# Kernel optimization log

Measured on AMD Instinct MI355X. Metric: run time of the kernel, lower is better.

The kernel has to match this reference:

```python
import jax, jax.numpy as jnp
import numpy as np

B, S, D = 2, 2048, 2048
NH, NKV = 32, 8
HD = D // NH          # 64
NREP = NH // NKV      # 4


def _rope(x, cos, sin):
    # x: [B, S, H, HD]; cos/sin: [S, HD//2]
    x2 = x.reshape(*x.shape[:-1], HD // 2, 2)
    x0, x1 = x2[..., 0], x2[..., 1]
    c = cos[None, :, None, :]
    s = sin[None, :, None, :]
    r0 = x0 * c - x1 * s
    r1 = x0 * s + x1 * c
    return jnp.stack([r0, r1], axis=-1).reshape(x.shape)


def setup_inputs() -> dict:
    key = jax.random.key(0)
    ks = jax.random.split(key, 5)
    x = jax.random.normal(ks[0], (B, S, D), dtype=jnp.float32)
    wq = jax.random.normal(ks[1], (D, NH * HD), dtype=jnp.float32) * (D ** -0.5)
    wk = jax.random.normal(ks[2], (D, NKV * HD), dtype=jnp.float32) * (D ** -0.5)
    wv = jax.random.normal(ks[3], (D, NKV * HD), dtype=jnp.float32) * (D ** -0.5)
    wo = jax.random.normal(ks[4], (NH * HD, D), dtype=jnp.float32) * (D ** -0.5)
    # standard RoPE frequencies: theta = 10000^(-2i/HD)
    inv_freq = 1.0 / (10000.0 ** (np.arange(0, HD, 2, dtype=np.float32) / HD))
    angles = np.arange(S, dtype=np.float32)[:, None] * inv_freq[None, :]  # [S, HD/2]
    freqs_cos = jnp.asarray(np.cos(angles))
    freqs_sin = jnp.asarray(np.sin(angles))
    return {"x": x, "freqs_cos": freqs_cos, "freqs_sin": freqs_sin,
            "wq": wq, "wk": wk, "wv": wv, "wo": wo}


def reference(x, freqs_cos, freqs_sin, wq, wk, wv, wo):
    b, s, _ = x.shape
    xq = (x @ wq).reshape(b, s, NH, HD)
    xk = (x @ wk).reshape(b, s, NKV, HD)
    xv = (x @ wv).reshape(b, s, NKV, HD)
    xq = _rope(xq, freqs_cos, freqs_sin)
    xk = _rope(xk, freqs_cos, freqs_sin)
    # GQA repeat_kv: expand kv heads to NH
    keys = jnp.repeat(xk, NREP, axis=2)    # [B, S, NH, HD]
    values = jnp.repeat(xv, NREP, axis=2)
    scores = jnp.einsum('bqhd,bkhd->bhqk', xq, keys) / jnp.sqrt(jnp.float32(HD))
    causal = jnp.tril(jnp.ones((s, s), dtype=bool))
    scores = jnp.where(causal[None, None], scores, -jnp.inf)
    attn = jax.nn.softmax(scores.astype(jnp.float32), axis=-1).astype(xq.dtype)
    out = jnp.einsum('bhqk,bkhd->bqhd', attn, values).reshape(b, s, NH * HD)
    return out @ wo
```

## Files before the change

kernel.cpp:

```cpp
#include <hip/hip_runtime.h>
#include <hip/hip_bf16.h>

#define S_LEN 2048
#define DMODEL 2048
#define N_H 32
#define N_KV 8
#define H_D 64
#define ROWS 4096
#define QKV_LD 3072

typedef __bf16 bf16x8 __attribute__((ext_vector_type(8)));
typedef float f32x4 __attribute__((ext_vector_type(4)));

static __device__ __forceinline__ unsigned short f2bf(float f) {
  unsigned int u = __float_as_uint(f);
  u += 0x7FFFu + ((u >> 16) & 1u);
  return (unsigned short)(u >> 16);
}
static __device__ __forceinline__ unsigned short f2bf_tr(float f) {
  return (unsigned short)(__float_as_uint(f) >> 16);
}
static __device__ __forceinline__ float bf2f(unsigned short s) {
  return __uint_as_float((unsigned int)s << 16);
}

static __device__ __forceinline__ void async16(const void* g, void* l) {
  __builtin_amdgcn_global_load_lds(
      (const __attribute__((address_space(1))) unsigned int*)g,
      (__attribute__((address_space(3))) unsigned int*)l, 16, 0, 0);
}

__global__ __launch_bounds__(256) void cvt_bf16_k(
    const float* __restrict__ in, unsigned short* __restrict__ out) {
  const size_t i = ((size_t)blockIdx.x * 256 + threadIdx.x) * 8;
  const float4 a = *(const float4*)&in[i];
  const float4 b = *(const float4*)&in[i + 4];
  union { unsigned short u[8]; uint4 v; } p;
  p.u[0] = f2bf(a.x); p.u[1] = f2bf(a.y); p.u[2] = f2bf(a.z); p.u[3] = f2bf(a.w);
  p.u[4] = f2bf(b.x); p.u[5] = f2bf(b.y); p.u[6] = f2bf(b.z); p.u[7] = f2bf(b.w);
  *(uint4*)&out[i] = p.v;
}

__global__ __launch_bounds__(256) void prep_all_k(
    const float* __restrict__ x, const float* __restrict__ wq,
    const float* __restrict__ wk, const float* __restrict__ wv,
    const float* __restrict__ wo, unsigned short* __restrict__ xb,
    unsigned short* __restrict__ wqkvT, unsigned short* __restrict__ woT) {
  const int z = blockIdx.z;
  if (z == 4) {
    const size_t i =
        (((size_t)blockIdx.y * 64 + blockIdx.x) * 256 + threadIdx.x) * 8;
    const float4 a = *(const float4*)&x[i];
    const float4 b = *(const float4*)&x[i + 4];
    union { unsigned short u[8]; uint4 v; } p;
    p.u[0] = f2bf(a.x); p.u[1] = f2bf(a.y); p.u[2] = f2bf(a.z); p.u[3] = f2bf(a.w);
    p.u[4] = f2bf(b.x); p.u[5] = f2bf(b.y); p.u[6] = f2bf(b.z); p.u[7] = f2bf(b.w);
    *(uint4*)&xb[i] = p.v;
    return;
  }
  const float* in;
  unsigned short* out;
  int C;
  if (z == 0)      { in = wq; out = wqkvT;                  C = 2048; }
  else if (z == 1) { in = wk; out = wqkvT + 2048ull * 2048; C = 512;  }
  else if (z == 2) { in = wv; out = wqkvT + 2560ull * 2048; C = 512;  }
  else             { in = wo; out = woT;                    C = 2048; }
  if (blockIdx.x * 32 >= C) return;

  __shared__ unsigned short tile[32][33];
  const int tx = threadIdx.x & 31;
  const int ty = threadIdx.x >> 5;
  const int r0 = blockIdx.y * 32;
  const int c0 = blockIdx.x * 32;
#pragma unroll
  for (int i = 0; i < 32; i += 8)
    tile[ty + i][tx] = f2bf(in[(size_t)(r0 + ty + i) * C + c0 + tx]);
  __syncthreads();
#pragma unroll
  for (int i = 0; i < 32; i += 8)
    out[(size_t)(c0 + ty + i) * 2048 + r0 + tx] = tile[tx][ty + i];
}

#define SCALE_LOG2E 0.18033688011112042f

__global__ __launch_bounds__(256) void rope_vt_k(
    unsigned short* __restrict__ qkv, unsigned short* __restrict__ vT,
    const float* __restrict__ fc, const float* __restrict__ fs) {
  const int blk = blockIdx.x;
  if (blk < 20480) {
    const int PQ = ROWS * N_H * (H_D / 2);
    const int PK = ROWS * N_KV * (H_D / 2);
    const int idx = blk * 256 + threadIdx.x;
    if (idx >= PQ + PK) return;
    unsigned short* base;
    float c, sn;
    bool isq;
    if (idx < PQ) {
      const int i = idx & 31;
      const int h = (idx >> 5) & 31;
      const int row = idx >> 10;
      const int s = row & (S_LEN - 1);
      c = fc[s * 32 + i];
      sn = fs[s * 32 + i];
      base = qkv + (size_t)row * QKV_LD + h * H_D + 2 * i;
      isq = true;
    } else {
      const int p = idx - PQ;
      const int i = p & 31;
      const int h = (p >> 5) & 7;
      const int row = p >> 8;
      const int s = row & (S_LEN - 1);
      c = fc[s * 32 + i];
      sn = fs[s * 32 + i];
      base = qkv + (size_t)row * QKV_LD + 2048 + h * H_D + 2 * i;
      isq = false;
    }
    const float x0 = bf2f(base[0]);
    const float x1 = bf2f(base[1]);
    const float sc = isq ? SCALE_LOG2E : 1.0f;
    base[0] = f2bf((x0 * c - x1 * sn) * sc);
    base[1] = f2bf((x0 * sn + x1 * c) * sc);
  } else {
    __shared__ unsigned short tile[32][33];
    const int t = blk - 20480;
    const int bx = t & 15;
    const int by = t >> 4;
    const unsigned short* in = qkv + 2560;
    const int tx = threadIdx.x & 31;
    const int ty = threadIdx.x >> 5;
    const int r0 = by * 32;
    const int c0 = bx * 32;
#pragma unroll
    for (int i = 0; i < 32; i += 8)
      tile[ty + i][tx] = in[(size_t)(r0 + ty + i) * QKV_LD + c0 + tx];
    __syncthreads();
#pragma unroll
    for (int i = 0; i < 32; i += 8)
      vT[(size_t)(c0 + ty + i) * ROWS + r0 + tx] = tile[tx][ty + i];
  }
}

template <int STORE_BF16>
__global__ __launch_bounds__(256) void gemm_bt_k(
    const unsigned short* __restrict__ A, const unsigned short* __restrict__ BT,
    void* __restrict__ Cp, int M, int N, int K, int lda) {
  __shared__ __align__(16) unsigned short As[128 * 32];
  __shared__ __align__(16) unsigned short Bs[128 * 32];
  const int tid = threadIdx.x;
  const int wave = tid >> 6;
  const int lane = tid & 63;
  const int quad = lane >> 4;
  const int l16 = lane & 15;
  const int m0 = blockIdx.x * 128;
  const int n0 = blockIdx.y * 128;
  const int wm = (wave >> 1) * 64;
  const int wn = (wave & 1) * 64;
  const int rsub = lane >> 2;
  const int coff = (lane & 3) * 8;
  f32x4 acc[4][4] = {};

  for (int kt = 0; kt < K; kt += 32) {
    __syncthreads();
#pragma unroll
    for (int t = 0; t < 2; t++) {
      const int row = wave * 32 + t * 16 + rsub;
      async16(&A[(size_t)(m0 + row) * lda + kt + coff],
              &As[(wave * 32 + t * 16) * 32]);
      async16(&BT[(size_t)(n0 + row) * K + kt + coff],
              &Bs[(wave * 32 + t * 16) * 32]);
    }
    __syncthreads();
    bf16x8 af[4], bfr[4];
#pragma unroll
    for (int i = 0; i < 4; i++)
      af[i] = *(const bf16x8*)&As[(wm + i * 16 + l16) * 32 + quad * 8];
#pragma unroll
    for (int j = 0; j < 4; j++)
      bfr[j] = *(const bf16x8*)&Bs[(wn + j * 16 + l16) * 32 + quad * 8];
#pragma unroll
    for (int i = 0; i < 4; i++)
#pragma unroll
      for (int j = 0; j < 4; j++)
        acc[i][j] =
            __builtin_amdgcn_mfma_f32_16x16x32_bf16(af[i], bfr[j], acc[i][j], 0, 0, 0);
  }

#pragma unroll
  for (int i = 0; i < 4; i++) {
#pragma unroll
    for (int e = 0; e < 4; e++) {
      const int mrow = m0 + wm + i * 16 + quad * 4 + e;
#pragma unroll
      for (int j = 0; j < 4; j++) {
        const int ncol = n0 + wn + j * 16 + l16;
        const float val = acc[i][j][e];
        if (STORE_BF16) {
          ((unsigned short*)Cp)[(size_t)mrow * N + ncol] = f2bf(val);
        } else {
          ((float*)Cp)[(size_t)mrow * N + ncol] = val;
        }
      }
    }
  }
}

template <int AF32, int STORE_BF16>
__global__ __launch_bounds__(256) void gemm_k(
    const void* __restrict__ Ap, const float* __restrict__ B,
    void* __restrict__ Cp, int M, int N, int K) {
  constexpr int LDP = 40;
  __shared__ __align__(16) unsigned short As[128 * LDP];
  __shared__ __align__(16) unsigned short Bs[128 * LDP];
  const int tid = threadIdx.x;
  const int wave = tid >> 6;
  const int lane = tid & 63;
  const int quad = lane >> 4;
  const int l16 = lane & 15;
  const int m0 = blockIdx.x * 128;
  const int n0 = blockIdx.y * 128;
  const int wm = (wave >> 1) * 64;
  const int wn = (wave & 1) * 64;
  f32x4 acc[4][4] = {};

  for (int kt = 0; kt < K; kt += 32) {
    __syncthreads();
    if (AF32) {
      const float* A = (const float*)Ap;
      for (int c = tid; c < 1024; c += 256) {
        const int r = c >> 3;
        const int cc = (c & 7) << 2;
        const float4 w = *(const float4*)&A[(size_t)(m0 + r) * K + kt + cc];
        union { unsigned short u[4]; uint2 v; } p;
        p.u[0] = f2bf(w.x); p.u[1] = f2bf(w.y);
        p.u[2] = f2bf(w.z); p.u[3] = f2bf(w.w);
        *(uint2*)&As[r * LDP + cc] = p.v;
      }
    } else {
      const unsigned short* A = (const unsigned short*)Ap;
      for (int c = tid; c < 512; c += 256) {
        const int r = c >> 2;
        const int cc = (c & 3) << 3;
        *(uint4*)&As[r * LDP + cc] =
            *(const uint4*)&A[(size_t)(m0 + r) * K + kt + cc];
      }
    }
    for (int c = tid; c < 1024; c += 256) {
      const int kr = c >> 5;
      const int nc = (c & 31) << 2;
      const float4 w = *(const float4*)&B[(size_t)(kt + kr) * N + n0 + nc];
      Bs[(nc + 0) * LDP + kr] = f2bf(w.x);
      Bs[(nc + 1) * LDP + kr] = f2bf(w.y);
      Bs[(nc + 2) * LDP + kr] = f2bf(w.z);
      Bs[(nc + 3) * LDP + kr] = f2bf(w.w);
    }
    __syncthreads();
    bf16x8 af[4], bfr[4];
#pragma unroll
    for (int i = 0; i < 4; i++)
      af[i] = *(const bf16x8*)&As[(wm + i * 16 + l16) * LDP + quad * 8];
#pragma unroll
    for (int j = 0; j < 4; j++)
      bfr[j] = *(const bf16x8*)&Bs[(wn + j * 16 + l16) * LDP + quad * 8];
#pragma unroll
    for (int i = 0; i < 4; i++)
#pragma unroll
      for (int j = 0; j < 4; j++)
        acc[i][j] =
            __builtin_amdgcn_mfma_f32_16x16x32_bf16(af[i], bfr[j], acc[i][j], 0, 0, 0);
  }
#pragma unroll
  for (int i = 0; i < 4; i++) {
#pragma unroll
    for (int e = 0; e < 4; e++) {
      const int mrow = m0 + wm + i * 16 + quad * 4 + e;
#pragma unroll
      for (int j = 0; j < 4; j++) {
        const int ncol = n0 + wn + j * 16 + l16;
        const float val = acc[i][j][e];
        if (STORE_BF16) {
          ((unsigned short*)Cp)[(size_t)mrow * N + ncol] = f2bf(val);
        } else {
          ((float*)Cp)[(size_t)mrow * N + ncol] = val;
        }
      }
    }
  }
}

__global__ __launch_bounds__(256) void rope_k(
    unsigned short* __restrict__ q, unsigned short* __restrict__ kk,
    const float* __restrict__ fc, const float* __restrict__ fs,
    int qstride, int kstride) {
  const int PQ = ROWS * N_H * (H_D / 2);
  const int PK = ROWS * N_KV * (H_D / 2);
  const int idx = blockIdx.x * 256 + threadIdx.x;
  if (idx >= PQ + PK) return;
  unsigned short* base;
  float c, sn;
  if (idx < PQ) {
    const int i = idx & 31;
    const int h = (idx >> 5) & 31;
    const int row = idx >> 10;
    const int s = row & (S_LEN - 1);
    c = fc[s * 32 + i];
    sn = fs[s * 32 + i];
    base = q + (size_t)row * qstride + h * H_D + 2 * i;
  } else {
    const int p = idx - PQ;
    const int i = p & 31;
    const int h = (p >> 5) & 7;
    const int row = p >> 8;
    const int s = row & (S_LEN - 1);
    c = fc[s * 32 + i];
    sn = fs[s * 32 + i];
    base = kk + (size_t)row * kstride + h * H_D + 2 * i;
  }
  const float x0 = bf2f(base[0]);
  const float x1 = bf2f(base[1]);
  base[0] = f2bf(x0 * c - x1 * sn);
  base[1] = f2bf(x0 * sn + x1 * c);
}

#define LK 72

__global__ __launch_bounds__(256) void attn_mfma6_k(
    const unsigned short* __restrict__ qkv, const unsigned short* __restrict__ vT,
    unsigned short* __restrict__ ao) {
  const int pair = blockIdx.x, h = blockIdx.y, b = blockIdx.z;
  const int hk = h >> 2;
  const int tid = threadIdx.x;
  const int wave = tid >> 6;
  const int l16 = tid & 15;
  const int quad = (tid & 63) >> 4;
  const int rr = tid >> 2;
  const int dc = (tid & 3) * 16;

  __shared__ __align__(16) unsigned short Ks[2][64 * LK];
  __shared__ __align__(16) unsigned short Vt[2][64 * LK];
  __shared__ __align__(16) unsigned short Ps[4][32 * LK];

  bf16x8 ones;
#pragma unroll
  for (int j = 0; j < 8; j++) ones[j] = (__bf16)1.0f;

  const size_t kbase =
      (size_t)(b * S_LEN) * QKV_LD + 2048 + hk * H_D + dc;
  const size_t vbase = (size_t)(hk * H_D + rr) * ROWS + b * S_LEN + dc;

  for (int sel = 0; sel < 2; ++sel) {
    const int qb = sel ? (15 - pair) : pair;
    const int row0 = qb * 128;
    const int ktiles = 2 * qb + 2;

    bf16x8 af[2][2];
#pragma unroll
    for (int r = 0; r < 2; r++) {
      const size_t qrow =
          (size_t)(b * S_LEN + row0 + wave * 32 + r * 16 + l16);
#pragma unroll
      for (int c = 0; c < 2; c++)
        af[r][c] =
            *(const bf16x8*)&qkv[qrow * QKV_LD + h * H_D + c * 32 + quad * 8];
    }

    f32x4 o_acc[2][4] = {};
    f32x4 l_acc[2] = {};

    uint4 rk0, rk1, rv0, rv1;
    {
      const size_t kro = kbase + (size_t)rr * QKV_LD;
      rk0 = *(const uint4*)&qkv[kro];
      rk1 = *(const uint4*)&qkv[kro + 8];
      rv0 = *(const uint4*)&vT[vbase];
      rv1 = *(const uint4*)&vT[vbase + 8];
    }
    __syncthreads();
    *(uint4*)&Ks[0][rr * LK + dc] = rk0;
    *(uint4*)&Ks[0][rr * LK + dc + 8] = rk1;
    *(uint4*)&Vt[0][rr * LK + dc] = rv0;
    *(uint4*)&Vt[0][rr * LK + dc + 8] = rv1;

    int cur = 0;
    for (int kt = 0; kt < ktiles; ++kt) {
      if (kt + 1 < ktiles) {
        const size_t kro = kbase + (size_t)((kt + 1) * 64 + rr) * QKV_LD;
        rk0 = *(const uint4*)&qkv[kro];
        rk1 = *(const uint4*)&qkv[kro + 8];
        const size_t vro = vbase + (size_t)(kt + 1) * 64;
        rv0 = *(const uint4*)&vT[vro];
        rv1 = *(const uint4*)&vT[vro + 8];
      }
      __syncthreads();

      f32x4 sacc[2][4];
#pragma unroll
      for (int n = 0; n < 4; n++) {
        f32x4 z0 = {}, z1 = {};
#pragma unroll
        for (int c = 0; c < 2; c++) {
          const bf16x8 bk =
              *(const bf16x8*)&Ks[cur][(n * 16 + l16) * LK + c * 32 + quad * 8];
          z0 = __builtin_amdgcn_mfma_f32_16x16x32_bf16(af[0][c], bk, z0, 0, 0, 0);
          z1 = __builtin_amdgcn_mfma_f32_16x16x32_bf16(af[1][c], bk, z1, 0, 0, 0);
        }
        sacc[0][n] = z0;
        sacc[1][n] = z1;
      }

      const bool maybe_mask = (kt >= 2 * qb);
      const int krel0 = (kt - 2 * qb) * 64;
#pragma unroll
      for (int r = 0; r < 2; r++) {
        const int qrel = wave * 32 + r * 16 + quad * 4;
        if (maybe_mask) {
#pragma unroll
          for (int n = 0; n < 4; n++)
#pragma unroll
            for (int e = 0; e < 4; e++) {
              float pe = exp2f(sacc[r][n][e]);
              if ((krel0 + n * 16 + l16) > (qrel + e)) pe = 0.f;
              Ps[wave][(r * 16 + quad * 4 + e) * LK + n * 16 + l16] =
                  f2bf_tr(pe);
            }
        } else {
#pragma unroll
          for (int n = 0; n < 4; n++)
#pragma unroll
            for (int e = 0; e < 4; e++)
              Ps[wave][(r * 16 + quad * 4 + e) * LK + n * 16 + l16] =
                  f2bf_tr(exp2f(sacc[r][n][e]));
        }
      }

      bf16x8 pf[2][2];
#pragma unroll
      for (int r = 0; r < 2; r++)
#pragma unroll
        for (int c = 0; c < 2; c++)
          pf[r][c] = *(const bf16x8*)&Ps[wave][(r * 16 + l16) * LK + c * 32 +
                                              quad * 8];
#pragma unroll
      for (int c = 0; c < 2; c++) {
        l_acc[0] = __builtin_amdgcn_mfma_f32_16x16x32_bf16(pf[0][c], ones,
                                                           l_acc[0], 0, 0, 0);
        l_acc[1] = __builtin_amdgcn_mfma_f32_16x16x32_bf16(pf[1][c], ones,
                                                           l_acc[1], 0, 0, 0);
      }
#pragma unroll
      for (int n = 0; n < 4; n++)
#pragma unroll
        for (int c = 0; c < 2; c++) {
          const bf16x8 bv =
              *(const bf16x8*)&Vt[cur][(n * 16 + l16) * LK + c * 32 + quad * 8];
          o_acc[0][n] =
              __builtin_amdgcn_mfma_f32_16x16x32_bf16(pf[0][c], bv, o_acc[0][n], 0, 0, 0);
          o_acc[1][n] =
              __builtin_amdgcn_mfma_f32_16x16x32_bf16(pf[1][c], bv, o_acc[1][n], 0, 0, 0);
        }

      if (kt + 1 < ktiles) {
        const int nxt = cur ^ 1;
        *(uint4*)&Ks[nxt][rr * LK + dc] = rk0;
        *(uint4*)&Ks[nxt][rr * LK + dc + 8] = rk1;
        *(uint4*)&Vt[nxt][rr * LK + dc] = rv0;
        *(uint4*)&Vt[nxt][rr * LK + dc + 8] = rv1;
      }
      cur ^= 1;
    }

#pragma unroll
    for (int r = 0; r < 2; r++)
#pragma unroll
      for (int e = 0; e < 4; e++) {
        const float inv = 1.f / l_acc[r][e];
        const size_t row = (size_t)(b * S_LEN + row0 + wave * 32 + r * 16 +
                                    quad * 4 + e);
#pragma unroll
        for (int n = 0; n < 4; n++)
          ao[row * QKV_LD + h * H_D + n * 16 + l16] =
              f2bf(o_acc[r][n][e] * inv);
      }
  }
}

__global__ __launch_bounds__(256) void attn_mfma_k(
    const unsigned short* __restrict__ q, const unsigned short* __restrict__ k,
    const unsigned short* __restrict__ v, unsigned short* __restrict__ ao) {
  const int qt = blockIdx.x, h = blockIdx.y, b = blockIdx.z;
  const int hk = h >> 2;
  const int tid = threadIdx.x;
  const int wave = tid >> 6;
  const int l16 = tid & 15;
  const int quad = (tid & 63) >> 4;

  __shared__ __align__(16) unsigned short Ks[64 * LK];
  __shared__ __align__(16) unsigned short Vt[64 * LK];
  __shared__ __align__(16) unsigned short Ps[64 * LK];

  bf16x8 af[2];
  {
    const size_t qrow = (size_t)(b * S_LEN + qt * 64 + wave * 16 + l16);
#pragma unroll
    for (int c = 0; c < 2; c++)
      af[c] = *(const bf16x8*)&q[qrow * DMODEL + h * H_D + c * 32 + quad * 8];
  }

  f32x4 o_acc[4] = {};
  float m_i[4], l_i[4];
#pragma unroll
  for (int e = 0; e < 4; e++) { m_i[e] = -INFINITY; l_i[e] = 0.f; }

  for (int kt = 0; kt <= qt; ++kt) {
    const int kb = kt * 64;
    __syncthreads();
    {
      const int kr = tid >> 2;
      const int dc = (tid & 3) * 16;
      const size_t gro = (size_t)(b * S_LEN + kb + kr) * (N_KV * H_D) + hk * H_D + dc;
      *(uint4*)&Ks[kr * LK + dc] = *(const uint4*)&k[gro];
      *(uint4*)&Ks[kr * LK + dc + 8] = *(const uint4*)&k[gro + 8];
      union { unsigned short u[8]; uint4 v; } w0, w1;
      w0.v = *(const uint4*)&v[gro];
      w1.v = *(const uint4*)&v[gro + 8];
#pragma unroll
      for (int j = 0; j < 8; j++) Vt[(dc + j) * LK + kr] = w0.u[j];
#pragma unroll
      for (int j = 0; j < 8; j++) Vt[(dc + 8 + j) * LK + kr] = w1.u[j];
    }
    __syncthreads();

    f32x4 sacc[4];
#pragma unroll
    for (int n = 0; n < 4; n++) {
      f32x4 z = {};
#pragma unroll
      for (int c = 0; c < 2; c++) {
        const bf16x8 bk = *(const bf16x8*)&Ks[(n * 16 + l16) * LK + c * 32 + quad * 8];
        z = __builtin_amdgcn_mfma_f32_16x16x32_bf16(af[c], bk, z, 0, 0, 0);
      }
      sacc[n] = z;
    }

    float p[4][4], mnew[4];
#pragma unroll
    for (int e = 0; e < 4; e++) mnew[e] = m_i[e];
#pragma unroll
    for (int n = 0; n < 4; n++)
#pragma unroll
      for (int e = 0; e < 4; e++) {
        float s = sacc[n][e] * 0.125f;
        if (kt == qt && (n * 16 + l16) > (wave * 16 + quad * 4 + e))
          s = -INFINITY;
        p[n][e] = s;
        mnew[e] = fmaxf(mnew[e], s);
      }
#pragma unroll
    for (int e = 0; e < 4; e++) {
      mnew[e] = fmaxf(mnew[e], __shfl_xor(mnew[e], 1));
      mnew[e] = fmaxf(mnew[e], __shfl_xor(mnew[e], 2));
      mnew[e] = fmaxf(mnew[e], __shfl_xor(mnew[e], 4));
      mnew[e] = fmaxf(mnew[e], __shfl_xor(mnew[e], 8));
      const float alpha = __expf(m_i[e] - mnew[e]);
      m_i[e] = mnew[e];
      l_i[e] *= alpha;
#pragma unroll
      for (int n = 0; n < 4; n++) o_acc[n][e] *= alpha;
    }
#pragma unroll
    for (int n = 0; n < 4; n++)
#pragma unroll
      for (int e = 0; e < 4; e++) {
        const float pe = __expf(p[n][e] - m_i[e]);
        p[n][e] = pe;
        l_i[e] += pe;
      }

#pragma unroll
    for (int n = 0; n < 4; n++)
#pragma unroll
      for (int e = 0; e < 4; e++)
        Ps[(wave * 16 + quad * 4 + e) * LK + n * 16 + l16] = f2bf(p[n][e]);
    __syncthreads();

    bf16x8 pf[2];
#pragma unroll
    for (int c = 0; c < 2; c++)
      pf[c] = *(const bf16x8*)&Ps[(wave * 16 + l16) * LK + c * 32 + quad * 8];
#pragma unroll
    for (int n = 0; n < 4; n++)
#pragma unroll
      for (int c = 0; c < 2; c++) {
        const bf16x8 bv = *(const bf16x8*)&Vt[(n * 16 + l16) * LK + c * 32 + quad * 8];
        o_acc[n] = __builtin_amdgcn_mfma_f32_16x16x32_bf16(pf[c], bv, o_acc[n], 0, 0, 0);
      }
  }

#pragma unroll
  for (int e = 0; e < 4; e++) {
    l_i[e] += __shfl_xor(l_i[e], 1);
    l_i[e] += __shfl_xor(l_i[e], 2);
    l_i[e] += __shfl_xor(l_i[e], 4);
    l_i[e] += __shfl_xor(l_i[e], 8);
    const float inv = 1.f / l_i[e];
    const size_t row = (size_t)(b * S_LEN + qt * 64 + wave * 16 + quad * 4 + e);
#pragma unroll
    for (int n = 0; n < 4; n++)
      ao[row * DMODEL + h * H_D + n * 16 + l16] = f2bf(o_acc[n][e] * inv);
  }
}

extern "C" void kernel_launch(void* const* d_in, const int* in_sizes, int n_in,
                              void* d_out, int out_size, void* d_ws, size_t ws_size,
                              hipStream_t stream) {
  const float* x = (const float*)d_in[0];
  const float* fc = (const float*)d_in[1];
  const float* fs = (const float*)d_in[2];
  const float* wq = (const float*)d_in[3];
  const float* wk = (const float*)d_in[4];
  const float* wv = (const float*)d_in[5];
  const float* wo = (const float*)d_in[6];

  char* ws = (char*)d_ws;
  const dim3 b256(256);

  if (ws_size >= (64ull << 20)) {
    unsigned short* qkv = (unsigned short*)(ws);
    unsigned short* xb = (unsigned short*)(ws + (24ull << 20));
    unsigned short* wqkvT = (unsigned short*)(ws + (40ull << 20));
    unsigned short* woT = (unsigned short*)(ws + (52ull << 20));
    unsigned short* vT = (unsigned short*)(ws + (60ull << 20));

    prep_all_k<<<dim3(64, 64, 5), b256, 0, stream>>>(x, wq, wk, wv, wo, xb,
                                                     wqkvT, woT);

    gemm_bt_k<1><<<dim3(32, 24), b256, 0, stream>>>(xb, wqkvT, qkv, 4096, 3072,
                                                    2048, 2048);

    rope_vt_k<<<dim3(20480 + 2048), b256, 0, stream>>>(qkv, vT, fc, fs);

    attn_mfma6_k<<<dim3(8, N_H, 2), b256, 0, stream>>>(qkv, vT, qkv);

    gemm_bt_k<0><<<dim3(32, 16), b256, 0, stream>>>(qkv, woT, d_out, 4096, 2048,
                                                    2048, QKV_LD);
  } else {
    unsigned short* q = (unsigned short*)(ws);
    unsigned short* k = (unsigned short*)(ws + (16ull << 20));
    unsigned short* v = (unsigned short*)(ws + (20ull << 20));
    unsigned short* xb = (unsigned short*)(ws + (24ull << 20));
    const bool have_xb = ws_size >= (40ull << 20);

    if (have_xb) {
      cvt_bf16_k<<<dim3(ROWS * DMODEL / (256 * 8)), b256, 0, stream>>>(x, xb);
      gemm_k<0, 1><<<dim3(32, 16), b256, 0, stream>>>(xb, wq, q, 4096, 2048, 2048);
      gemm_k<0, 1><<<dim3(32, 4), b256, 0, stream>>>(xb, wk, k, 4096, 512, 2048);
      gemm_k<0, 1><<<dim3(32, 4), b256, 0, stream>>>(xb, wv, v, 4096, 512, 2048);
    } else {
      gemm_k<1, 1><<<dim3(32, 16), b256, 0, stream>>>(x, wq, q, 4096, 2048, 2048);
      gemm_k<1, 1><<<dim3(32, 4), b256, 0, stream>>>(x, wk, k, 4096, 512, 2048);
      gemm_k<1, 1><<<dim3(32, 4), b256, 0, stream>>>(x, wv, v, 4096, 512, 2048);
    }

    rope_k<<<dim3(20480), b256, 0, stream>>>(q, k, fc, fs, N_H * H_D, N_KV * H_D);
    attn_mfma_k<<<dim3(S_LEN / 64, N_H, 2), b256, 0, stream>>>(q, k, v, q);
    gemm_k<0, 0><<<dim3(32, 16), b256, 0, stream>>>(q, wo, d_out, 4096, 2048, 2048);
  }
}
```

Before: 325.4 us.

## Load V fragments directly from global in attention; double K-step in GEMM

The attention kernel no longer stages V^T through shared memory. Each wave loads its MFMA B-operand fragments for V straight from global (the V tiles are shared by the four query heads of a KV group and should hit cache), which removes the LDS writes and reads for V and shrinks the LDS footprint. The GEMM now loads two 32-wide K slices per barrier pair, halving the number of __syncthreads per K sweep at the cost of twice the LDS per block. The risks are more uncoalesced global traffic and exposed global latency in the attention inner loop, and lower occupancy in the GEMM.

Result: no change. 329.2 us (+1.2%).

```diff
diff --git a/kernel.cpp b/kernel.cpp
--- a/kernel.cpp
+++ b/kernel.cpp
@@ -144,8 +144,8 @@
 __global__ __launch_bounds__(256) void gemm_bt_k(
     const unsigned short* __restrict__ A, const unsigned short* __restrict__ BT,
     void* __restrict__ Cp, int M, int N, int K, int lda) {
-  __shared__ __align__(16) unsigned short As[128 * 32];
-  __shared__ __align__(16) unsigned short Bs[128 * 32];
+  __shared__ __align__(16) unsigned short As[2][128 * 32];
+  __shared__ __align__(16) unsigned short Bs[2][128 * 32];
   const int tid = threadIdx.x;
   const int wave = tid >> 6;
   const int lane = tid & 63;
@@ -159,30 +159,36 @@
   const int coff = (lane & 3) * 8;
   f32x4 acc[4][4] = {};
 
-  for (int kt = 0; kt < K; kt += 32) {
-    __syncthreads();
-#pragma unroll
-    for (int t = 0; t < 2; t++) {
-      const int row = wave * 32 + t * 16 + rsub;
-      async16(&A[(size_t)(m0 + row) * lda + kt + coff],
-              &As[(wave * 32 + t * 16) * 32]);
-      async16(&BT[(size_t)(n0 + row) * K + kt + coff],
-              &Bs[(wave * 32 + t * 16) * 32]);
-    }
-    __syncthreads();
-    bf16x8 af[4], bfr[4];
-#pragma unroll
-    for (int i = 0; i < 4; i++)
-      af[i] = *(const bf16x8*)&As[(wm + i * 16 + l16) * 32 + quad * 8];
-#pragma unroll
-    for (int j = 0; j < 4; j++)
-      bfr[j] = *(const bf16x8*)&Bs[(wn + j * 16 + l16) * 32 + quad * 8];
-#pragma unroll
-    for (int i = 0; i < 4; i++)
+  for (int kt = 0; kt < K; kt += 64) {
+    __syncthreads();
+#pragma unroll
+    for (int hh = 0; hh < 2; hh++) {
+#pragma unroll
+      for (int t = 0; t < 2; t++) {
+        const int row = wave * 32 + t * 16 + rsub;
+        async16(&A[(size_t)(m0 + row) * lda + kt + hh * 32 + coff],
+                &As[hh][(wave * 32 + t * 16) * 32]);
+        async16(&BT[(size_t)(n0 + row) * K + kt + hh * 32 + coff],
+                &Bs[hh][(wave * 32 + t * 16) * 32]);
+      }
+    }
+    __syncthreads();
+#pragma unroll
+    for (int hh = 0; hh < 2; hh++) {
+      bf16x8 af[4], bfr[4];
+#pragma unroll
+      for (int i = 0; i < 4; i++)
+        af[i] = *(const bf16x8*)&As[hh][(wm + i * 16 + l16) * 32 + quad * 8];
 #pragma unroll
       for (int j = 0; j < 4; j++)
-        acc[i][j] =
-            __builtin_amdgcn_mfma_f32_16x16x32_bf16(af[i], bfr[j], acc[i][j], 0, 0, 0);
+        bfr[j] = *(const bf16x8*)&Bs[hh][(wn + j * 16 + l16) * 32 + quad * 8];
+#pragma unroll
+      for (int i = 0; i < 4; i++)
+#pragma unroll
+        for (int j = 0; j < 4; j++)
+          acc[i][j] = __builtin_amdgcn_mfma_f32_16x16x32_bf16(af[i], bfr[j],
+                                                              acc[i][j], 0, 0, 0);
+    }
   }
 
 #pragma unroll
@@ -323,7 +329,7 @@
 
 #define LK 72
 
-__global__ __launch_bounds__(256) void attn_mfma6_k(
+__global__ __launch_bounds__(256) void attn_mfma7_k(
     const unsigned short* __restrict__ qkv, const unsigned short* __restrict__ vT,
     unsigned short* __restrict__ ao) {
   const int pair = blockIdx.x, h = blockIdx.y, b = blockIdx.z;
@@ -336,7 +342,6 @@
   const int dc = (tid & 3) * 16;
 
   __shared__ __align__(16) unsigned short Ks[2][64 * LK];
-  __shared__ __align__(16) unsigned short Vt[2][64 * LK];
   __shared__ __align__(16) unsigned short Ps[4][32 * LK];
 
   bf16x8 ones;
@@ -345,7 +350,7 @@
 
   const size_t kbase =
       (size_t)(b * S_LEN) * QKV_LD + 2048 + hk * H_D + dc;
-  const size_t vbase = (size_t)(hk * H_D + rr) * ROWS + b * S_LEN + dc;
+  const size_t vfbase = (size_t)(hk * H_D + l16) * ROWS + b * S_LEN + quad * 8;
 
   for (int sel = 0; sel < 2; ++sel) {
     const int qb = sel ? (15 - pair) : pair;
@@ -366,30 +371,31 @@
     f32x4 o_acc[2][4] = {};
     f32x4 l_acc[2] = {};
 
-    uint4 rk0, rk1, rv0, rv1;
+    uint4 rk0, rk1;
     {
       const size_t kro = kbase + (size_t)rr * QKV_LD;
       rk0 = *(const uint4*)&qkv[kro];
       rk1 = *(const uint4*)&qkv[kro + 8];
-      rv0 = *(const uint4*)&vT[vbase];
-      rv1 = *(const uint4*)&vT[vbase + 8];
     }
     __syncthreads();
     *(uint4*)&Ks[0][rr * LK + dc] = rk0;
     *(uint4*)&Ks[0][rr * LK + dc + 8] = rk1;
-    *(uint4*)&Vt[0][rr * LK + dc] = rv0;
-    *(uint4*)&Vt[0][rr * LK + dc + 8] = rv1;
 
     int cur = 0;
     for (int kt = 0; kt < ktiles; ++kt) {
+      const int kb = kt * 64;
       if (kt + 1 < ktiles) {
         const size_t kro = kbase + (size_t)((kt + 1) * 64 + rr) * QKV_LD;
         rk0 = *(const uint4*)&qkv[kro];
         rk1 = *(const uint4*)&qkv[kro + 8];
-        const size_t vro = vbase + (size_t)(kt + 1) * 64;
-        rv0 = *(const uint4*)&vT[vro];
-        rv1 = *(const uint4*)&vT[vro + 8];
-      }
+      }
+      bf16x8 bv[4][2];
+#pragma unroll
+      for (int n = 0; n < 4; n++)
+#pragma unroll
+        for (int c = 0; c < 2; c++)
+          bv[n][c] =
+              *(const bf16x8*)&vT[vfbase + (size_t)(n * 16) * ROWS + kb + c * 32];
       __syncthreads();
 
       f32x4 sacc[2][4];
@@ -450,20 +456,16 @@
       for (int n = 0; n < 4; n++)
 #pragma unroll
         for (int c = 0; c < 2; c++) {
-          const bf16x8 bv =
-              *(const bf16x8*)&Vt[cur][(n * 16 + l16) * LK + c * 32 + quad * 8];
-          o_acc[0][n] =
-              __builtin_amdgcn_mfma_f32_16x16x32_bf16(pf[0][c], bv, o_acc[0][n], 0, 0, 0);
-          o_acc[1][n] =
-              __builtin_amdgcn_mfma_f32_16x16x32_bf16(pf[1][c], bv, o_acc[1][n], 0, 0, 0);
+          o_acc[0][n] = __builtin_amdgcn_mfma_f32_16x16x32_bf16(
+              pf[0][c], bv[n][c], o_acc[0][n], 0, 0, 0);
+          o_acc[1][n] = __builtin_amdgcn_mfma_f32_16x16x32_bf16(
+              pf[1][c], bv[n][c], o_acc[1][n], 0, 0, 0);
         }
 
       if (kt + 1 < ktiles) {
         const int nxt = cur ^ 1;
         *(uint4*)&Ks[nxt][rr * LK + dc] = rk0;
         *(uint4*)&Ks[nxt][rr * LK + dc + 8] = rk1;
-        *(uint4*)&Vt[nxt][rr * LK + dc] = rv0;
-        *(uint4*)&Vt[nxt][rr * LK + dc + 8] = rv1;
       }
       cur ^= 1;
     }
@@ -638,7 +640,7 @@
 
     rope_vt_k<<<dim3(20480 + 2048), b256, 0, stream>>>(qkv, vT, fc, fs);
 
-    attn_mfma6_k<<<dim3(8, N_H, 2), b256, 0, stream>>>(qkv, vT, qkv);
+    attn_mfma7_k<<<dim3(8, N_H, 2), b256, 0, stream>>>(qkv, vT, qkv);
 
     gemm_bt_k<0><<<dim3(32, 16), b256, 0, stream>>>(qkv, woT, d_out, 4096, 2048,
                                                     2048, QKV_LD);
```
